# Kernel optimization log

Hardware: AMD Instinct MI355X
Metric: run time of the kernel (lower is better)

Reference implementation:

```python
import jax, jax.numpy as jnp
import numpy as np

HID = 256
POS_FREQ = 10
DIR_FREQ = 4
POS_ENC = 3 * (2 * POS_FREQ + 1)   # 63
DIR_ENC = 3 * (2 * DIR_FREQ + 1)   # 27
N_PTS = 262144


def _posenc(x, num_freq):
    freqs = (2.0 ** jnp.arange(num_freq)).astype(x.dtype)      # [F]
    xf = x[..., None, :] * freqs[:, None]                       # [..., F, D]
    sc = jnp.stack([jnp.sin(xf), jnp.cos(xf)], axis=-2)         # [..., F, 2, D]
    return jnp.concatenate([x, sc.reshape(*x.shape[:-1], -1)], axis=-1)


def _linear_init(key, fan_in, fan_out):
    kw, kb = jax.random.split(key)
    s = 1.0 / np.sqrt(fan_in)
    W = jax.random.uniform(kw, (fan_in, fan_out), jnp.float32, -s, s)
    b = jax.random.uniform(kb, (fan_out,), jnp.float32, -s, s)
    return W, b


def setup_inputs() -> dict:
    key = jax.random.key(0)
    ks = jax.random.split(key, 16)
    inp = {
        "positions": jax.random.normal(ks[0], (N_PTS, 3), jnp.float32),
        "directions": jax.random.normal(ks[1], (N_PTS, 3), jnp.float32),
    }
    W, b = _linear_init(ks[2], POS_ENC, HID)
    inp["W_in"], inp["b_in"] = W, b
    # 7 hidden layers; layer index 4 takes skip concat (HID + POS_ENC)
    for i in range(7):
        fan_in = HID + POS_ENC if i == 4 else HID
        W, b = _linear_init(ks[3 + i], fan_in, HID)
        inp[f"W_h{i}"], inp[f"b_h{i}"] = W, b
    W, b = _linear_init(ks[10], HID, HID + 1)
    inp["W_out"], inp["b_out"] = W, b
    W, b = _linear_init(ks[11], HID + DIR_ENC, HID // 2)
    inp["W_r1"], inp["b_r1"] = W, b
    W, b = _linear_init(ks[12], HID // 2, 3)
    inp["W_r2"], inp["b_r2"] = W, b
    return inp


def _forward(positions, directions, W_in, b_in, hidden_params, W_out, b_out,
             W_r1, b_r1, W_r2, b_r2):
    pe = _posenc(positions, POS_FREQ)    # [N, 63]
    de = _posenc(directions, DIR_FREQ)   # [N, 27]
    h = jax.nn.relu(pe @ W_in + b_in)    # [N, 256]
    for i, (W, b) in enumerate(hidden_params):
        if i == 4:
            h = jnp.concatenate([h, pe], axis=-1)  # skip connection [N, 319]
        h = jax.nn.relu(h @ W + b)
    out = h @ W_out + b_out                      # [N, 257]
    features = out[..., :HID]                    # [N, 256]
    density = jax.nn.relu(out[..., HID:HID + 1])  # [N, 1]
    rgb_in = jnp.concatenate([features, de], axis=-1)  # [N, 283]
    rgb = jax.nn.sigmoid(jax.nn.relu(rgb_in @ W_r1 + b_r1) @ W_r2 + b_r2)  # [N, 3]
    return rgb, density


def reference(positions, directions, W_in, b_in,
              W_h0, b_h0, W_h1, b_h1, W_h2, b_h2, W_h3, b_h3,
              W_h4, b_h4, W_h5, b_h5, W_h6, b_h6,
              W_out, b_out, W_r1, b_r1, W_r2, b_r2):
    hidden = [(W_h0, b_h0), (W_h1, b_h1), (W_h2, b_h2), (W_h3, b_h3),
              (W_h4, b_h4), (W_h5, b_h5), (W_h6, b_h6)]
    return _forward(positions, directions, W_in, b_in, hidden,
                    W_out, b_out, W_r1, b_r1, W_r2, b_r2)
```

## Files before the change

kernel.cpp:

```cpp
#include <hip/hip_runtime.h>
#include <math.h>

#define NPTS 262144
#define MT 128

typedef __attribute__((ext_vector_type(8))) short bf16x8;
typedef __attribute__((ext_vector_type(4))) float f32x4;
typedef __attribute__((ext_vector_type(16))) float f32x16;
typedef __attribute__((ext_vector_type(2))) unsigned int u32x2;

#if defined(__has_builtin)
#if __has_builtin(__builtin_amdgcn_cvt_pk_bf16_f32)
#define HAVE_CVT_PK_BF16 1
#endif
#endif

__device__ __forceinline__ short f2bf(float f) {
    union { float f; unsigned u; } v; v.f = f;
    unsigned r = v.u + 0x7fffu + ((v.u >> 16) & 1u);
    return (short)(r >> 16);
}
__device__ __forceinline__ unsigned pk2(float a, float b) {
#ifdef HAVE_CVT_PK_BF16
    auto r = __builtin_amdgcn_cvt_pk_bf16_f32(a, b);
    unsigned u; __builtin_memcpy(&u, &r, 4);
    return u;
#else
    return ((unsigned)(unsigned short)f2bf(a)) |
           ((unsigned)(unsigned short)f2bf(b) << 16);
#endif
}

#define OFF_IN   0
#define SZ_IN    (64*256)
#define OFF_H0   (OFF_IN + SZ_IN)
#define SZ_H     (256*256)
#define OFF_H1   (OFF_H0 + SZ_H)
#define OFF_H2   (OFF_H1 + SZ_H)
#define OFF_H3   (OFF_H2 + SZ_H)
#define OFF_H4   (OFF_H3 + SZ_H)
#define SZ_H4    (320*256)
#define OFF_H5   (OFF_H4 + SZ_H4)
#define OFF_H6   (OFF_H5 + SZ_H)
#define OFF_OUT  (OFF_H6 + SZ_H)
#define SZ_OUTM  (256*256)
#define OFF_OUTD (OFF_OUT + SZ_OUTM)
#define SZ_OUTD  (256*16)
#define OFF_R1   (OFF_OUTD + SZ_OUTD)
#define SZ_R1    (288*128)
#define OFF_R2   (OFF_R1 + SZ_R1)
#define SZ_R2    (128*16)
#define WS_TOTAL (OFF_R2 + SZ_R2)

struct PrepP { const float* W[11]; short* ws; };

__global__ __launch_bounds__(256) void prep_all(PrepP pp) {
    int i = blockIdx.x * 256 + threadIdx.x;
    if (i >= WS_TOTAL) return;
    const int offs[13] = {OFF_IN, OFF_H0, OFF_H1, OFF_H2, OFF_H3, OFF_H4,
                          OFF_H5, OFF_H6, OFF_OUT, OFF_OUTD, OFF_R1, OFF_R2,
                          WS_TOTAL};
    const int wsrc[12] = {0,1,2,3,4,5,6,7,8,8,9,10};
    const int Ks[12]   = {63,256,256,256,256,319,256,256,256,256,283,128};
    const int Nsrc[12] = {256,256,256,256,256,256,256,256,257,257,128,3};
    int seg = 0;
    while (i >= offs[seg + 1]) seg++;
    int li = i - offs[seg];
    int j = li & 7, L = (li >> 3) & 63, tile = li >> 9;
    const float* W = pp.W[wsrc[seg]];
    float v = 0.f;
    if (seg == 9) {
        int k = tile * 32 + ((L >> 4) << 3) + j;
        if (k < 256 && (L & 15) == 0) v = W[k * 257 + 256];
    } else if (seg == 11) {
        int k = tile * 32 + ((L >> 4) << 3) + j;
        int n = L & 15;
        if (k < 128 && n < 3) v = W[k * 3 + n];
    } else {
        int nNb = (seg == 10) ? 4 : 8;
        int nb = tile % nNb, kt = tile / nNb;
        int k = kt * 16 + ((L >> 5) << 3) + j;
        int n = nb * 32 + (L & 31);
        if (k < Ks[seg]) v = W[k * Nsrc[seg] + n];
    }
    pp.ws[i] = f2bf(v);
}

struct Params {
    const float *pos, *dir;
    const float *b_in, *b_h0, *b_h1, *b_h2, *b_h3, *b_h4, *b_h5, *b_h6;
    const float *b_out, *b_r1, *b_r2;
    const short *w;
    float *out;
};

template<int NKT, int NNB, int TM, int MODE>
__device__ __forceinline__ void layer32(const short* __restrict__ Wsw,
                                        const short* __restrict__ Wd,
                                        const float* __restrict__ bias,
                                        short* X, float* dout, int p0,
                                        int nb, int mbB, int wave, int lane) {
    const int l31 = lane & 31, hi = lane >> 5;
    const short* xb = X + hi * 1024 + (mbB * 32 + l31) * 8;
    const short* wp = Wsw + (size_t)(nb * 64 + lane) * 8;

    bf16x8 a0 = *(const bf16x8*)(wp);
    bf16x8 a1 = *(const bf16x8*)(wp + (size_t)NNB * 512);

    __syncthreads();

    if (MODE == 1) {
        const int l15 = lane & 15, quad = lane >> 4;
        const short* xd = X + quad * 1024 + (wave * 16 + l15) * 8;
        f32x4 ad = (f32x4){0.f, 0.f, 0.f, 0.f};
#pragma unroll
        for (int kt = 0; kt < 8; ++kt) {
            bf16x8 b = *(const bf16x8*)(xd + kt * 4096);
            bf16x8 a = *(const bf16x8*)(Wd + (size_t)(kt * 64 + lane) * 8);
            ad = __builtin_amdgcn_mfma_f32_16x16x32_bf16(a, b, ad, 0, 0, 0);
        }
        if (quad == 0)
            dout[3 * NPTS + p0 + wave * 16 + l15] = fmaxf(ad[0] + bias[256], 0.f);
    }

    f32x16 acc[TM];
#pragma unroll
    for (int t = 0; t < TM; t++)
#pragma unroll
        for (int r = 0; r < 16; r++) acc[t][r] = 0.f;

    bf16x8 b_c[TM];
#pragma unroll
    for (int t = 0; t < TM; t++)
        b_c[t] = *(const bf16x8*)(xb + t * 256);

#pragma unroll
    for (int kt = 0; kt < NKT; ++kt) {
        bf16x8 b_n[TM], a_n;
        if (kt + 1 < NKT) {
#pragma unroll
            for (int t = 0; t < TM; t++)
                b_n[t] = *(const bf16x8*)(xb + (kt + 1) * 2048 + t * 256);
        }
        if (kt + 2 < NKT)
            a_n = *(const bf16x8*)(wp + (size_t)(kt + 2) * NNB * 512);
        if ((kt & 1) == 0) {
#pragma unroll
            for (int t = 0; t < TM; t++)
                acc[t] = __builtin_amdgcn_mfma_f32_32x32x16_bf16(a0, b_c[t], acc[t], 0, 0, 0);
        } else {
#pragma unroll
            for (int t = 0; t < TM; t++)
                acc[t] = __builtin_amdgcn_mfma_f32_32x32x16_bf16(a1, b_c[t], acc[t], 0, 0, 0);
        }
        if (kt + 2 < NKT) {
            if ((kt & 1) == 0) a0 = a_n; else a1 = a_n;
        }
        if (kt + 1 < NKT) {
#pragma unroll
            for (int t = 0; t < TM; t++) b_c[t] = b_n[t];
        }
    }

    __syncthreads();

#pragma unroll
    for (int t = 0; t < TM; t++) {
        const int m = (mbB + t) * 32 + l31;
#pragma unroll
        for (int rq = 0; rq < 4; rq++) {
            const int nbase = nb * 32 + rq * 8 + hi * 4;
            const f32x4 bv = *(const f32x4*)(bias + nbase);
            float v0 = acc[t][rq * 4 + 0] + bv[0];
            float v1 = acc[t][rq * 4 + 1] + bv[1];
            float v2 = acc[t][rq * 4 + 2] + bv[2];
            float v3 = acc[t][rq * 4 + 3] + bv[3];
            if (MODE == 0) {
                v0 = fmaxf(v0, 0.f); v1 = fmaxf(v1, 0.f);
                v2 = fmaxf(v2, 0.f); v3 = fmaxf(v3, 0.f);
            }
            u32x2 w; w[0] = pk2(v0, v1); w[1] = pk2(v2, v3);
            *(u32x2*)(X + (size_t)(nb * 4 + rq) * 1024 + m * 8 + hi * 4) = w;
        }
    }
}

__global__ __launch_bounds__(512, 4) void nerf_fused(Params P) {
    __shared__ __align__(16) short X[40 * 1024];
    const int tid = threadIdx.x;
    const int wave = tid >> 6, lane = tid & 63;
    const int p0 = blockIdx.x * MT;

    for (int i = tid; i < 128 * 8; i += 512) {
        const int pt = i & 127, g = i >> 7;
        const float x0 = P.pos[(p0 + pt) * 3 + 0];
        const float x1 = P.pos[(p0 + pt) * 3 + 1];
        const float x2 = P.pos[(p0 + pt) * 3 + 2];
        bf16x8 v;
#pragma unroll
        for (int j = 0; j < 8; j++) {
            const int d = g * 8 + j;
            float val = 0.f;
            if (d < 3) val = (d == 0) ? x0 : (d == 1) ? x1 : x2;
            else if (d < 63) {
                const int e = d - 3, f = e / 6, r = e % 6;
                const float x = (r % 3 == 0) ? x0 : (r % 3 == 1) ? x1 : x2;
                const float xf = x * (float)(1 << f);
                val = (r < 3) ? sinf(xf) : cosf(xf);
            }
            v[j] = f2bf(val);
        }
        *(bf16x8*)(X + ((size_t)g * 128 + pt) * 8) = v;
        *(bf16x8*)(X + ((size_t)(32 + g) * 128 + pt) * 8) = v;
    }

    bf16x8 de_v;
    const int ptD = tid & 127, gD = tid >> 7;
    {
        const float x0 = P.dir[(p0 + ptD) * 3 + 0];
        const float x1 = P.dir[(p0 + ptD) * 3 + 1];
        const float x2 = P.dir[(p0 + ptD) * 3 + 2];
#pragma unroll
        for (int j = 0; j < 8; j++) {
            const int d = gD * 8 + j;
            float val = 0.f;
            if (d < 3) val = (d == 0) ? x0 : (d == 1) ? x1 : x2;
            else if (d < 27) {
                const int e = d - 3, f = e / 6, r = e % 6;
                const float x = (r % 3 == 0) ? x0 : (r % 3 == 1) ? x1 : x2;
                const float xf = x * (float)(1 << f);
                val = (r < 3) ? sinf(xf) : cosf(xf);
            }
            de_v[j] = f2bf(val);
        }
    }

    layer32< 4, 8, 4, 0>(P.w + OFF_IN, nullptr, P.b_in, X, P.out, p0, wave, 0, wave, lane);
    layer32<16, 8, 4, 0>(P.w + OFF_H0, nullptr, P.b_h0, X, P.out, p0, wave, 0, wave, lane);
    layer32<16, 8, 4, 0>(P.w + OFF_H1, nullptr, P.b_h1, X, P.out, p0, wave, 0, wave, lane);
    layer32<16, 8, 4, 0>(P.w + OFF_H2, nullptr, P.b_h2, X, P.out, p0, wave, 0, wave, lane);
    layer32<16, 8, 4, 0>(P.w + OFF_H3, nullptr, P.b_h3, X, P.out, p0, wave, 0, wave, lane);
    layer32<20, 8, 4, 0>(P.w + OFF_H4, nullptr, P.b_h4, X, P.out, p0, wave, 0, wave, lane);

    *(bf16x8*)(X + ((size_t)(32 + gD) * 128 + ptD) * 8) = de_v;

    layer32<16, 8, 4, 0>(P.w + OFF_H5, nullptr, P.b_h5, X, P.out, p0, wave, 0, wave, lane);
    layer32<16, 8, 4, 0>(P.w + OFF_H6, nullptr, P.b_h6, X, P.out, p0, wave, 0, wave, lane);
    layer32<16, 8, 4, 1>(P.w + OFF_OUT, P.w + OFF_OUTD, P.b_out, X, P.out, p0, wave, 0, wave, lane);

    layer32<18, 4, 2, 0>(P.w + OFF_R1, nullptr, P.b_r1, X, P.out, p0, wave & 3, (wave >> 2) * 2, wave, lane);

    __syncthreads();
    {
        const int l15 = lane & 15, quad = lane >> 4;
        f32x4 acc = (f32x4){0.f, 0.f, 0.f, 0.f};
        const short* xb = X + quad * 1024 + (wave * 16 + l15) * 8;
#pragma unroll
        for (int kt = 0; kt < 4; ++kt) {
            bf16x8 b = *(const bf16x8*)(xb + kt * 4096);
            bf16x8 a = *(const bf16x8*)(P.w + OFF_R2 + (size_t)(kt * 64 + lane) * 8);
            acc = __builtin_amdgcn_mfma_f32_16x16x32_bf16(a, b, acc, 0, 0, 0);
        }
        if (quad == 0) {
#pragma unroll
            for (int r = 0; r < 3; r++) {
                const float v = acc[r] + P.b_r2[r];
                P.out[(size_t)(p0 + wave * 16 + l15) * 3 + r] = 1.f / (1.f + expf(-v));
            }
        }
    }
}

extern "C" void kernel_launch(void* const* d_in, const int* in_sizes, int n_in,
                              void* d_out, int out_size, void* d_ws, size_t ws_size,
                              hipStream_t stream) {
    short* ws = (short*)d_ws;

    PrepP pp;
    pp.W[0]  = (const float*)d_in[2];
    pp.W[1]  = (const float*)d_in[4];
    pp.W[2]  = (const float*)d_in[6];
    pp.W[3]  = (const float*)d_in[8];
    pp.W[4]  = (const float*)d_in[10];
    pp.W[5]  = (const float*)d_in[12];
    pp.W[6]  = (const float*)d_in[14];
    pp.W[7]  = (const float*)d_in[16];
    pp.W[8]  = (const float*)d_in[18];
    pp.W[9]  = (const float*)d_in[20];
    pp.W[10] = (const float*)d_in[22];
    pp.ws = ws;
    hipLaunchKernelGGL(prep_all, dim3((WS_TOTAL + 255) / 256), dim3(256), 0, stream, pp);

    Params P;
    P.pos  = (const float*)d_in[0];
    P.dir  = (const float*)d_in[1];
    P.b_in = (const float*)d_in[3];
    P.b_h0 = (const float*)d_in[5];
    P.b_h1 = (const float*)d_in[7];
    P.b_h2 = (const float*)d_in[9];
    P.b_h3 = (const float*)d_in[11];
    P.b_h4 = (const float*)d_in[13];
    P.b_h5 = (const float*)d_in[15];
    P.b_h6 = (const float*)d_in[17];
    P.b_out = (const float*)d_in[19];
    P.b_r1 = (const float*)d_in[21];
    P.b_r2 = (const float*)d_in[23];
    P.w = ws;
    P.out = (float*)d_out;
    hipLaunchKernelGGL(nerf_fused, dim3(NPTS / MT), dim3(512), 0, stream, P);
}
```

Measured before the change: 402.6 us.

## Prefetch next layer's weight fragments and use LDS-only barriers

Each layer now issues the global loads for the first two weight fragments of the next layer and passes them out through references. Work no longer stalls on a fresh global load at the start of every layer. The full __syncthreads is replaced by a barrier that waits only on LDS counters, so those prefetched global loads stay in flight across barriers. This costs extra registers for the carried fragments, which could affect occupancy under the 512x4 launch bounds.

```diff
diff --git a/kernel.cpp b/kernel.cpp
--- a/kernel.cpp
+++ b/kernel.cpp
@@ -29,6 +29,11 @@
     return ((unsigned)(unsigned short)f2bf(a)) |
            ((unsigned)(unsigned short)f2bf(b) << 16);
 #endif
+}
+
+__device__ __forceinline__ void barrier_lds() {
+    asm volatile("s_waitcnt lgkmcnt(0)" ::: "memory");
+    __builtin_amdgcn_s_barrier();
 }
 
 #define OFF_IN   0
@@ -99,15 +104,19 @@
                                         const short* __restrict__ Wd,
                                         const float* __restrict__ bias,
                                         short* X, float* dout, int p0,
-                                        int nb, int mbB, int wave, int lane) {
+                                        int nb, int mbB, int wave, int lane,
+                                        bf16x8& a0io, bf16x8& a1io,
+                                        const short* __restrict__ wpn, int nnbn) {
     const int l31 = lane & 31, hi = lane >> 5;
     const short* xb = X + hi * 1024 + (mbB * 32 + l31) * 8;
     const short* wp = Wsw + (size_t)(nb * 64 + lane) * 8;
 
-    bf16x8 a0 = *(const bf16x8*)(wp);
-    bf16x8 a1 = *(const bf16x8*)(wp + (size_t)NNB * 512);
-
-    __syncthreads();
+    bf16x8 na0 = *(const bf16x8*)(wpn);
+    bf16x8 na1 = *(const bf16x8*)(wpn + (size_t)nnbn * 512);
+
+    bf16x8 a0 = a0io, a1 = a1io;
+
+    barrier_lds();
 
     if (MODE == 1) {
         const int l15 = lane & 15, quad = lane >> 4;
@@ -162,7 +171,7 @@
         }
     }
 
-    __syncthreads();
+    barrier_lds();
 
 #pragma unroll
     for (int t = 0; t < TM; t++) {
@@ -183,6 +192,8 @@
             *(u32x2*)(X + (size_t)(nb * 4 + rq) * 1024 + m * 8 + hi * 4) = w;
         }
     }
+
+    a0io = na0; a1io = na1;
 }
 
 __global__ __launch_bounds__(512, 4) void nerf_fused(Params P) {
@@ -190,6 +201,13 @@
     const int tid = threadIdx.x;
     const int wave = tid >> 6, lane = tid & 63;
     const int p0 = blockIdx.x * MT;
+
+    const size_t fo    = (size_t)(wave * 64 + lane) * 8;
+    const size_t fo_r1 = (size_t)((wave & 3) * 64 + lane) * 8;
+    const size_t fo_r2 = (size_t)lane * 8;
+
+    bf16x8 a0 = *(const bf16x8*)(P.w + OFF_IN + fo);
+    bf16x8 a1 = *(const bf16x8*)(P.w + OFF_IN + fo + 8 * 512);
 
     for (int i = tid; i < 128 * 8; i += 512) {
         const int pt = i & 127, g = i >> 7;
@@ -235,32 +253,36 @@
         }
     }
 
-    layer32< 4, 8, 4, 0>(P.w + OFF_IN, nullptr, P.b_in, X, P.out, p0, wave, 0, wave, lane);
-    layer32<16, 8, 4, 0>(P.w + OFF_H0, nullptr, P.b_h0, X, P.out, p0, wave, 0, wave, lane);
-    layer32<16, 8, 4, 0>(P.w + OFF_H1, nullptr, P.b_h1, X, P.out, p0, wave, 0, wave, lane);
-    layer32<16, 8, 4, 0>(P.w + OFF_H2, nullptr, P.b_h2, X, P.out, p0, wave, 0, wave, lane);
-    layer32<16, 8, 4, 0>(P.w + OFF_H3, nullptr, P.b_h3, X, P.out, p0, wave, 0, wave, lane);
-    layer32<20, 8, 4, 0>(P.w + OFF_H4, nullptr, P.b_h4, X, P.out, p0, wave, 0, wave, lane);
+    layer32< 4, 8, 4, 0>(P.w + OFF_IN, nullptr, P.b_in, X, P.out, p0, wave, 0, wave, lane, a0, a1, P.w + OFF_H0 + fo, 8);
+    layer32<16, 8, 4, 0>(P.w + OFF_H0, nullptr, P.b_h0, X, P.out, p0, wave, 0, wave, lane, a0, a1, P.w + OFF_H1 + fo, 8);
+    layer32<16, 8, 4, 0>(P.w + OFF_H1, nullptr, P.b_h1, X, P.out, p0, wave, 0, wave, lane, a0, a1, P.w + OFF_H2 + fo, 8);
+    layer32<16, 8, 4, 0>(P.w + OFF_H2, nullptr, P.b_h2, X, P.out, p0, wave, 0, wave, lane, a0, a1, P.w + OFF_H3 + fo, 8);
+    layer32<16, 8, 4, 0>(P.w + OFF_H3, nullptr, P.b_h3, X, P.out, p0, wave, 0, wave, lane, a0, a1, P.w + OFF_H4 + fo, 8);
+    layer32<20, 8, 4, 0>(P.w + OFF_H4, nullptr, P.b_h4, X, P.out, p0, wave, 0, wave, lane, a0, a1, P.w + OFF_H5 + fo, 8);
 
     *(bf16x8*)(X + ((size_t)(32 + gD) * 128 + ptD) * 8) = de_v;
 
-    layer32<16, 8, 4, 0>(P.w + OFF_H5, nullptr, P.b_h5, X, P.out, p0, wave, 0, wave, lane);
-    layer32<16, 8, 4, 0>(P.w + OFF_H6, nullptr, P.b_h6, X, P.out, p0, wave, 0, wave, lane);
-    layer32<16, 8, 4, 1>(P.w + OFF_OUT, P.w + OFF_OUTD, P.b_out, X, P.out, p0, wave, 0, wave, lane);
-
-    layer32<18, 4, 2, 0>(P.w + OFF_R1, nullptr, P.b_r1, X, P.out, p0, wave & 3, (wave >> 2) * 2, wave, lane);
-
-    __syncthreads();
+    layer32<16, 8, 4, 0>(P.w + OFF_H5, nullptr, P.b_h5, X, P.out, p0, wave, 0, wave, lane, a0, a1, P.w + OFF_H6 + fo, 8);
+    layer32<16, 8, 4, 0>(P.w + OFF_H6, nullptr, P.b_h6, X, P.out, p0, wave, 0, wave, lane, a0, a1, P.w + OFF_OUT + fo, 8);
+    layer32<16, 8, 4, 1>(P.w + OFF_OUT, P.w + OFF_OUTD, P.b_out, X, P.out, p0, wave, 0, wave, lane, a0, a1, P.w + OFF_R1 + fo_r1, 4);
+
+    layer32<18, 4, 2, 0>(P.w + OFF_R1, nullptr, P.b_r1, X, P.out, p0, wave & 3, (wave >> 2) * 2, wave, lane, a0, a1, P.w + OFF_R2 + fo_r2, 1);
+
+    barrier_lds();
     {
         const int l15 = lane & 15, quad = lane >> 4;
+        const short* xb = X + quad * 1024 + (wave * 16 + l15) * 8;
+        bf16x8 a2 = *(const bf16x8*)(P.w + OFF_R2 + (size_t)(2 * 64 + lane) * 8);
+        bf16x8 a3 = *(const bf16x8*)(P.w + OFF_R2 + (size_t)(3 * 64 + lane) * 8);
         f32x4 acc = (f32x4){0.f, 0.f, 0.f, 0.f};
-        const short* xb = X + quad * 1024 + (wave * 16 + l15) * 8;
-#pragma unroll
-        for (int kt = 0; kt < 4; ++kt) {
-            bf16x8 b = *(const bf16x8*)(xb + kt * 4096);
-            bf16x8 a = *(const bf16x8*)(P.w + OFF_R2 + (size_t)(kt * 64 + lane) * 8);
-            acc = __builtin_amdgcn_mfma_f32_16x16x32_bf16(a, b, acc, 0, 0, 0);
-        }
+        bf16x8 b0 = *(const bf16x8*)(xb);
+        bf16x8 b1 = *(const bf16x8*)(xb + 4096);
+        bf16x8 b2 = *(const bf16x8*)(xb + 8192);
+        bf16x8 b3 = *(const bf16x8*)(xb + 12288);
+        acc = __builtin_amdgcn_mfma_f32_16x16x32_bf16(a0, b0, acc, 0, 0, 0);
+        acc = __builtin_amdgcn_mfma_f32_16x16x32_bf16(a1, b1, acc, 0, 0, 0);
+        acc = __builtin_amdgcn_mfma_f32_16x16x32_bf16(a2, b2, acc, 0, 0, 0);
+        acc = __builtin_amdgcn_mfma_f32_16x16x32_bf16(a3, b3, acc, 0, 0, 0);
         if (quad == 0) {
 #pragma unroll
             for (int r = 0; r < 3; r++) {
```

Result: no change. 403.7 us (+0.3%).
